# Optimization experiments

Measured on AMD Instinct MI355X. Metric: run time of the kernel, lower is better.

The kernel has to match this reference:

```python
import jax, jax.numpy as jnp
import numpy as np
from jax.ops import segment_sum

N_NODES = 100000


def _add_self_loops(edge_index, n):
    loop = jnp.arange(n, dtype=edge_index.dtype)
    src = jnp.concatenate([edge_index[0], loop])
    dst = jnp.concatenate([edge_index[1], loop])
    return src, dst


def _gcn_conv(x, W, b, src, dst, n):
    # PyG GCNConv: h = X W; out[i] = sum_j norm(j,i) h[j] + b, with self-loops
    h = x @ W                                             # [N, out]
    deg = segment_sum(jnp.ones_like(src, dtype=x.dtype), dst, num_segments=n)
    dinv = jnp.where(deg > 0, jax.lax.rsqrt(deg), 0.0)    # deg^{-1/2}
    norm = dinv[src] * dinv[dst]                          # [E]
    msg = h[src] * norm[:, None]                          # gather + scale
    out = segment_sum(msg, dst, num_segments=n)           # scatter-add
    return out + b


def setup_inputs() -> dict:
    key = jax.random.key(0)
    ks = jax.random.split(key, 8)
    x = jax.random.normal(ks[0], (N_NODES, 128), dtype=jnp.float32)
    edge_index = jax.random.randint(ks[1], (2, 600000), 0, N_NODES, dtype=jnp.int64)
    s1 = 1.0 / np.sqrt(128); s2 = 1.0 / np.sqrt(64); s3 = 1.0 / np.sqrt(32)
    return {
        "x": x,
        "edge_index": edge_index,
        "W1": jax.random.uniform(ks[2], (128, 64), jnp.float32, -s1, s1),
        "b1": jnp.zeros((64,), jnp.float32),
        "W2": jax.random.uniform(ks[3], (64, 32), jnp.float32, -s2, s2),
        "b2": jnp.zeros((32,), jnp.float32),
        "Wc": jax.random.uniform(ks[4], (32, 1), jnp.float32, -s3, s3),
        "bc": jnp.zeros((1,), jnp.float32),
    }


def reference(x, edge_index, W1, b1, W2, b2, Wc, bc):
    n = x.shape[0]
    src, dst = _add_self_loops(edge_index, n)
    h = jax.nn.relu(_gcn_conv(x, W1, b1, src, dst, n))
    h = jax.nn.relu(_gcn_conv(h, W2, b2, src, dst, n))
    return h @ Wc + bc
```

## Files before the change

### kernel.cpp

```cpp
#include <hip/hip_runtime.h>


#define SCAN_THREADS 256
#define SCAN_PER_T   8
#define SCAN_TILE    (SCAN_THREADS * SCAN_PER_T)

__global__ __launch_bounds__(256) void count_kernel(const int* __restrict__ dst,
                                                    int* __restrict__ deg, int E) {
    int e = blockIdx.x * blockDim.x + threadIdx.x;
    if (e < E) atomicAdd(&deg[dst[e]], 1);
}

__global__ __launch_bounds__(SCAN_THREADS) void tile_reduce_kernel(const int* __restrict__ deg,
                                                                   int* __restrict__ bsum,
                                                                   int n) {
    __shared__ int s[SCAN_THREADS];
    int t = threadIdx.x;
    int gbase = blockIdx.x * SCAN_TILE + t * SCAN_PER_T;
    int local = 0;
#pragma unroll
    for (int k = 0; k < SCAN_PER_T; ++k) {
        int i = gbase + k;
        if (i < n) local += deg[i];
    }
    s[t] = local;
    __syncthreads();
    for (int off = SCAN_THREADS / 2; off > 0; off >>= 1) {
        if (t < off) s[t] += s[t + off];
        __syncthreads();
    }
    if (t == 0) bsum[blockIdx.x] = s[0];
}

__global__ __launch_bounds__(SCAN_THREADS) void scan_bsums_kernel(int* __restrict__ bsum,
                                                                  int* __restrict__ row_ptr,
                                                                  int nb, int n) {
    __shared__ int s[SCAN_THREADS];
    int t = threadIdx.x;
    s[t] = (t < nb) ? bsum[t] : 0;
    __syncthreads();
    for (int off = 1; off < SCAN_THREADS; off <<= 1) {
        int v = (t >= off) ? s[t - off] : 0;
        __syncthreads();
        s[t] += v;
        __syncthreads();
    }
    if (t < nb) bsum[t] = (t == 0) ? 0 : s[t - 1];
    if (t == 0) row_ptr[n] = s[nb - 1];
}

__global__ __launch_bounds__(SCAN_THREADS) void tile_apply_kernel(int* __restrict__ deg,
                                                                  const int* __restrict__ bsum,
                                                                  int* __restrict__ row_ptr,
                                                                  float* __restrict__ dinv,
                                                                  int n) {
    __shared__ int s[SCAN_THREADS];
    int t = threadIdx.x;
    int gbase = blockIdx.x * SCAN_TILE + t * SCAN_PER_T;

    int d[SCAN_PER_T];
    int inc[SCAN_PER_T];
    int run = 0;
#pragma unroll
    for (int k = 0; k < SCAN_PER_T; ++k) {
        int i = gbase + k;
        d[k] = (i < n) ? deg[i] : 0;
        run += d[k];
        inc[k] = run;
    }
    s[t] = run;
    __syncthreads();
    for (int off = 1; off < SCAN_THREADS; off <<= 1) {
        int v = (t >= off) ? s[t - off] : 0;
        __syncthreads();
        s[t] += v;
        __syncthreads();
    }
    int base = bsum[blockIdx.x] + ((t == 0) ? 0 : s[t - 1]);
#pragma unroll
    for (int k = 0; k < SCAN_PER_T; ++k) {
        int i = gbase + k;
        if (i < n) {
            int ex = base + inc[k] - d[k];
            row_ptr[i] = ex;
            deg[i] = ex;
            dinv[i] = rsqrtf((float)(d[k] + 1));
        }
    }
}

__global__ __launch_bounds__(256) void fill_kernel(const int* __restrict__ src,
                                                   const int* __restrict__ dst,
                                                   int* __restrict__ cursor,
                                                   int* __restrict__ col, int E) {
    int e = blockIdx.x * blockDim.x + threadIdx.x;
    if (e < E) {
        int pos = atomicAdd(&cursor[dst[e]], 1);
        col[pos] = src[e];
    }
}

template <int IN, int OUT>
__global__ __launch_bounds__(512) void gemm_kernel(const float* __restrict__ X,
                                                   const float* __restrict__ W,
                                                   float* __restrict__ H, int n) {
    constexpr int STRIP = OUT / 4;
    __shared__ float Ws[IN * OUT];
    for (int i = threadIdx.x; i < IN * OUT / 4; i += blockDim.x)
        ((float4*)Ws)[i] = ((const float4*)W)[i];
    __syncthreads();

    int t = blockIdx.x * blockDim.x + threadIdx.x;
    int node = t >> 2;
    int strip = (t & 3) * STRIP;
    if (node >= n) return;

    float acc[STRIP];
#pragma unroll
    for (int j = 0; j < STRIP; ++j) acc[j] = 0.f;

    const float* xr = X + (size_t)node * IN;
#pragma unroll 4
    for (int k = 0; k < IN; k += 4) {
        float4 xv = *(const float4*)(xr + k);
        const float* w0 = Ws + (k + 0) * OUT + strip;
        const float* w1 = Ws + (k + 1) * OUT + strip;
        const float* w2 = Ws + (k + 2) * OUT + strip;
        const float* w3 = Ws + (k + 3) * OUT + strip;
#pragma unroll
        for (int j = 0; j < STRIP; j += 4) {
            float4 a = *(const float4*)(w0 + j);
            float4 b = *(const float4*)(w1 + j);
            float4 c = *(const float4*)(w2 + j);
            float4 dd = *(const float4*)(w3 + j);
            acc[j + 0] += xv.x * a.x + xv.y * b.x + xv.z * c.x + xv.w * dd.x;
            acc[j + 1] += xv.x * a.y + xv.y * b.y + xv.z * c.y + xv.w * dd.y;
            acc[j + 2] += xv.x * a.z + xv.y * b.z + xv.z * c.z + xv.w * dd.z;
            acc[j + 3] += xv.x * a.w + xv.y * b.w + xv.z * c.w + xv.w * dd.w;
        }
    }

    float* hr = H + (size_t)node * OUT + strip;
#pragma unroll
    for (int j = 0; j < STRIP; j += 4)
        *(float4*)(hr + j) = make_float4(acc[j], acc[j + 1], acc[j + 2], acc[j + 3]);
}

template <int F>
__global__ __launch_bounds__(256) void agg_relu_kernel(const int* __restrict__ row_ptr,
                                                       const int* __restrict__ col,
                                                       const float* __restrict__ dinv,
                                                       const float* __restrict__ H,
                                                       const float* __restrict__ b,
                                                       float* __restrict__ OUT, int n) {
    constexpr int TPE = F / 4;
    int t = blockIdx.x * blockDim.x + threadIdx.x;
    int node = t / TPE;
    int c = t % TPE;
    if (node >= n) return;
    int rs = row_ptr[node], re = row_ptr[node + 1];
    float di = dinv[node];
    float4 acc = make_float4(0.f, 0.f, 0.f, 0.f);
    int e = rs;
    for (; e + 1 < re; e += 2) {
        int s0 = col[e], s1 = col[e + 1];
        float w0 = dinv[s0], w1 = dinv[s1];
        float4 v0 = *(const float4*)(H + (size_t)s0 * F + c * 4);
        float4 v1 = *(const float4*)(H + (size_t)s1 * F + c * 4);
        acc.x += w0 * v0.x + w1 * v1.x;
        acc.y += w0 * v0.y + w1 * v1.y;
        acc.z += w0 * v0.z + w1 * v1.z;
        acc.w += w0 * v0.w + w1 * v1.w;
    }
    if (e < re) {
        int s0 = col[e];
        float w0 = dinv[s0];
        float4 v0 = *(const float4*)(H + (size_t)s0 * F + c * 4);
        acc.x += w0 * v0.x; acc.y += w0 * v0.y;
        acc.z += w0 * v0.z; acc.w += w0 * v0.w;
    }
    float4 hs = *(const float4*)(H + (size_t)node * F + c * 4);
    float4 bb = *(const float4*)(b + c * 4);
    float d2 = di * di;
    float4 r;
    r.x = di * acc.x + d2 * hs.x + bb.x;
    r.y = di * acc.y + d2 * hs.y + bb.y;
    r.z = di * acc.z + d2 * hs.z + bb.z;
    r.w = di * acc.w + d2 * hs.w + bb.w;
    r.x = r.x > 0.f ? r.x : 0.f;
    r.y = r.y > 0.f ? r.y : 0.f;
    r.z = r.z > 0.f ? r.z : 0.f;
    r.w = r.w > 0.f ? r.w : 0.f;
    *(float4*)(OUT + (size_t)node * F + c * 4) = r;
}

__global__ __launch_bounds__(256) void agg_final_kernel(const int* __restrict__ row_ptr,
                                                        const int* __restrict__ col,
                                                        const float* __restrict__ dinv,
                                                        const float* __restrict__ H,
                                                        const float* __restrict__ b2,
                                                        const float* __restrict__ Wc,
                                                        const float* __restrict__ bc,
                                                        float* __restrict__ out, int n) {
    constexpr int F = 32, TPE = 8;
    int t = blockIdx.x * blockDim.x + threadIdx.x;
    int node = t / TPE;
    int c = t % TPE;
    if (node >= n) return;
    int rs = row_ptr[node], re = row_ptr[node + 1];
    float di = dinv[node];
    float4 acc = make_float4(0.f, 0.f, 0.f, 0.f);
    int e = rs;
    for (; e + 1 < re; e += 2) {
        int s0 = col[e], s1 = col[e + 1];
        float w0 = dinv[s0], w1 = dinv[s1];
        float4 v0 = *(const float4*)(H + (size_t)s0 * F + c * 4);
        float4 v1 = *(const float4*)(H + (size_t)s1 * F + c * 4);
        acc.x += w0 * v0.x + w1 * v1.x;
        acc.y += w0 * v0.y + w1 * v1.y;
        acc.z += w0 * v0.z + w1 * v1.z;
        acc.w += w0 * v0.w + w1 * v1.w;
    }
    if (e < re) {
        int s0 = col[e];
        float w0 = dinv[s0];
        float4 v0 = *(const float4*)(H + (size_t)s0 * F + c * 4);
        acc.x += w0 * v0.x; acc.y += w0 * v0.y;
        acc.z += w0 * v0.z; acc.w += w0 * v0.w;
    }
    float4 hs = *(const float4*)(H + (size_t)node * F + c * 4);
    float4 bb = *(const float4*)(b2 + c * 4);
    float4 wc = *(const float4*)(Wc + c * 4);
    float d2 = di * di;
    float4 r;
    r.x = di * acc.x + d2 * hs.x + bb.x;
    r.y = di * acc.y + d2 * hs.y + bb.y;
    r.z = di * acc.z + d2 * hs.z + bb.z;
    r.w = di * acc.w + d2 * hs.w + bb.w;
    float dot = (r.x > 0.f ? r.x : 0.f) * wc.x + (r.y > 0.f ? r.y : 0.f) * wc.y +
                (r.z > 0.f ? r.z : 0.f) * wc.z + (r.w > 0.f ? r.w : 0.f) * wc.w;
    dot += __shfl_xor(dot, 1, 8);
    dot += __shfl_xor(dot, 2, 8);
    dot += __shfl_xor(dot, 4, 8);
    if (c == 0) out[node] = dot + bc[0];
}

extern "C" void kernel_launch(void* const* d_in, const int* in_sizes, int n_in,
                              void* d_out, int out_size, void* d_ws, size_t ws_size,
                              hipStream_t stream) {
    const float* x  = (const float*)d_in[0];
    const int*   ei = (const int*)d_in[1];
    const float* W1 = (const float*)d_in[2];
    const float* b1 = (const float*)d_in[3];
    const float* W2 = (const float*)d_in[4];
    const float* b2 = (const float*)d_in[5];
    const float* Wc = (const float*)d_in[6];
    const float* bc = (const float*)d_in[7];
    float* out = (float*)d_out;

    const int n = in_sizes[0] / 128;
    const int E = in_sizes[1] / 2;

    const int* src = ei;
    const int* dst = ei + (size_t)E;

    const int nb = (n + SCAN_TILE - 1) / SCAN_TILE;

    float* dinv    = (float*)d_ws;
    int*   deg     = (int*)d_ws + n;
    int*   row_ptr = (int*)d_ws + 2 * (size_t)n;
    int*   col     = row_ptr + (n + 1);
    int*   bsum    = col + E;
    float* bufA    = (float*)(bsum + 256);
    float* bufB    = bufA + (size_t)n * 64;

    hipMemsetAsync(deg, 0, (size_t)n * 4, stream);
    count_kernel<<<(E + 255) / 256, 256, 0, stream>>>(dst, deg, E);
    tile_reduce_kernel<<<nb, SCAN_THREADS, 0, stream>>>(deg, bsum, n);
    scan_bsums_kernel<<<1, SCAN_THREADS, 0, stream>>>(bsum, row_ptr, nb, n);
    tile_apply_kernel<<<nb, SCAN_THREADS, 0, stream>>>(deg, bsum, row_ptr, dinv, n);
    fill_kernel<<<(E + 255) / 256, 256, 0, stream>>>(src, dst, deg, col, E);

    gemm_kernel<128, 64><<<(n * 4 + 511) / 512, 512, 0, stream>>>(x, W1, bufA, n);
    agg_relu_kernel<64><<<(n * 16 + 255) / 256, 256, 0, stream>>>(row_ptr, col, dinv,
                                                                  bufA, b1, bufB, n);
    gemm_kernel<64, 32><<<(n * 4 + 511) / 512, 512, 0, stream>>>(bufB, W2, bufA, n);
    agg_final_kernel<<<(n * 8 + 255) / 256, 256, 0, stream>>>(row_ptr, col, dinv,
                                                              bufA, b2, Wc, bc, out, n);
}
```

Baseline: 271.9 us.

## Restructure GEMM to stage X tiles in LDS and read W via uniform loads

```diff
diff --git a/kernel.cpp b/kernel.cpp
--- a/kernel.cpp
+++ b/kernel.cpp
@@ -101,49 +101,72 @@
 }
 
 template <int IN, int OUT>
-__global__ __launch_bounds__(512) void gemm_kernel(const float* __restrict__ X,
+__global__ __launch_bounds__(256) void gemm_kernel(const float* __restrict__ X,
                                                    const float* __restrict__ W,
                                                    float* __restrict__ H, int n) {
-    constexpr int STRIP = OUT / 4;
-    __shared__ float Ws[IN * OUT];
-    for (int i = threadIdx.x; i < IN * OUT / 4; i += blockDim.x)
-        ((float4*)Ws)[i] = ((const float4*)W)[i];
-    __syncthreads();
-
-    int t = blockIdx.x * blockDim.x + threadIdx.x;
-    int node = t >> 2;
-    int strip = (t & 3) * STRIP;
-    if (node >= n) return;
-
-    float acc[STRIP];
-#pragma unroll
-    for (int j = 0; j < STRIP; ++j) acc[j] = 0.f;
-
-    const float* xr = X + (size_t)node * IN;
-#pragma unroll 4
-    for (int k = 0; k < IN; k += 4) {
-        float4 xv = *(const float4*)(xr + k);
-        const float* w0 = Ws + (k + 0) * OUT + strip;
-        const float* w1 = Ws + (k + 1) * OUT + strip;
-        const float* w2 = Ws + (k + 2) * OUT + strip;
-        const float* w3 = Ws + (k + 3) * OUT + strip;
-#pragma unroll
-        for (int j = 0; j < STRIP; j += 4) {
-            float4 a = *(const float4*)(w0 + j);
-            float4 b = *(const float4*)(w1 + j);
-            float4 c = *(const float4*)(w2 + j);
-            float4 dd = *(const float4*)(w3 + j);
-            acc[j + 0] += xv.x * a.x + xv.y * b.x + xv.z * c.x + xv.w * dd.x;
-            acc[j + 1] += xv.x * a.y + xv.y * b.y + xv.z * c.y + xv.w * dd.y;
-            acc[j + 2] += xv.x * a.z + xv.y * b.z + xv.z * c.z + xv.w * dd.z;
-            acc[j + 3] += xv.x * a.w + xv.y * b.w + xv.z * c.w + xv.w * dd.w;
+    constexpr int NB = 128;
+    constexpr int KT = 32;
+    constexpr int STRIDE = KT + 1;
+    constexpr int JW = OUT / 2;
+    constexpr int NKT = IN / KT;
+    constexpr int NF4 = NB * KT / 4;
+
+    __shared__ float Xs[NB * STRIDE];
+
+    const int t = threadIdx.x;
+    const int wv = __builtin_amdgcn_readfirstlane(t >> 6);
+    const int lane = t & 63;
+    const int node0 = blockIdx.x * NB;
+    const int lnode = ((wv >> 1) << 6) + lane;
+    const int jbase = (wv & 1) * JW;
+    const int node = node0 + lnode;
+
+    float acc[JW];
+#pragma unroll
+    for (int j = 0; j < JW; ++j) acc[j] = 0.f;
+
+    for (int kt = 0; kt < NKT; ++kt) {
+        __syncthreads();
+        for (int f = t; f < NF4; f += 256) {
+            int nd = f >> 3;
+            int kq = f & 7;
+            float4 val = make_float4(0.f, 0.f, 0.f, 0.f);
+            if (node0 + nd < n)
+                val = *(const float4*)(X + (size_t)(node0 + nd) * IN + kt * KT + kq * 4);
+            float* p = Xs + nd * STRIDE + kq * 4;
+            p[0] = val.x; p[1] = val.y; p[2] = val.z; p[3] = val.w;
         }
-    }
-
-    float* hr = H + (size_t)node * OUT + strip;
-#pragma unroll
-    for (int j = 0; j < STRIP; j += 4)
-        *(float4*)(hr + j) = make_float4(acc[j], acc[j + 1], acc[j + 2], acc[j + 3]);
+        __syncthreads();
+
+        const float* xrow = Xs + lnode * STRIDE;
+#pragma unroll
+        for (int kq = 0; kq < KT; kq += 4) {
+            float x0 = xrow[kq + 0];
+            float x1 = xrow[kq + 1];
+            float x2 = xrow[kq + 2];
+            float x3 = xrow[kq + 3];
+            const float* wr = W + (size_t)(kt * KT + kq) * OUT + jbase;
+#pragma unroll
+            for (int jg = 0; jg < JW; jg += 4) {
+                float4 w0 = *(const float4*)(wr + 0 * OUT + jg);
+                float4 w1 = *(const float4*)(wr + 1 * OUT + jg);
+                float4 w2 = *(const float4*)(wr + 2 * OUT + jg);
+                float4 w3 = *(const float4*)(wr + 3 * OUT + jg);
+                acc[jg + 0] += x0 * w0.x + x1 * w1.x + x2 * w2.x + x3 * w3.x;
+                acc[jg + 1] += x0 * w0.y + x1 * w1.y + x2 * w2.y + x3 * w3.y;
+                acc[jg + 2] += x0 * w0.z + x1 * w1.z + x2 * w2.z + x3 * w3.z;
+                acc[jg + 3] += x0 * w0.w + x1 * w1.w + x2 * w2.w + x3 * w3.w;
+            }
+        }
+    }
+
+    if (node < n) {
+        float* hr = H + (size_t)node * OUT + jbase;
+#pragma unroll
+        for (int jg = 0; jg < JW; jg += 4)
+            *(float4*)(hr + jg) =
+                make_float4(acc[jg], acc[jg + 1], acc[jg + 2], acc[jg + 3]);
+    }
 }
 
 template <int F>
@@ -281,10 +304,12 @@
     tile_apply_kernel<<<nb, SCAN_THREADS, 0, stream>>>(deg, bsum, row_ptr, dinv, n);
     fill_kernel<<<(E + 255) / 256, 256, 0, stream>>>(src, dst, deg, col, E);
 
-    gemm_kernel<128, 64><<<(n * 4 + 511) / 512, 512, 0, stream>>>(x, W1, bufA, n);
+    const int gemm_grid = (n + 127) / 128;
+
+    gemm_kernel<128, 64><<<gemm_grid, 256, 0, stream>>>(x, W1, bufA, n);
     agg_relu_kernel<64><<<(n * 16 + 255) / 256, 256, 0, stream>>>(row_ptr, col, dinv,
                                                                   bufA, b1, bufB, n);
-    gemm_kernel<64, 32><<<(n * 4 + 511) / 512, 512, 0, stream>>>(bufB, W2, bufA, n);
+    gemm_kernel<64, 32><<<gemm_grid, 256, 0, stream>>>(bufB, W2, bufA, n);
     agg_final_kernel<<<(n * 8 + 255) / 256, 256, 0, stream>>>(row_ptr, col, dinv,
                                                               bufA, b2, Wc, bc, out, n);
 }
```

After: 275.7 us. Within noise of the previous version (+1.4%).

## Replace per-node GEMM with shared-memory tiled register-blocked GEMM

Applied to the files above, without the earlier changes.

```diff
diff --git a/kernel.cpp b/kernel.cpp
--- a/kernel.cpp
+++ b/kernel.cpp
@@ -100,50 +100,71 @@
     }
 }
 
-template <int IN, int OUT>
-__global__ __launch_bounds__(512) void gemm_kernel(const float* __restrict__ X,
-                                                   const float* __restrict__ W,
-                                                   float* __restrict__ H, int n) {
-    constexpr int STRIP = OUT / 4;
+template <int IN, int OUT, int BM, int TM, int TN>
+__global__ __launch_bounds__(256) void gemm_tiled(const float* __restrict__ X,
+                                                  const float* __restrict__ W,
+                                                  float* __restrict__ H, int n) {
+    constexpr int BK = 32;
+    constexpr int XST = BK + 1;
+    constexpr int NTX = OUT / TN;
+    constexpr int NF4 = BM * BK / 4;
+    static_assert(NTX * (BM / TM) == 256, "thread mapping");
+
     __shared__ float Ws[IN * OUT];
-    for (int i = threadIdx.x; i < IN * OUT / 4; i += blockDim.x)
+    __shared__ float Xs[BM * XST];
+
+    const int t = threadIdx.x;
+    for (int i = t; i < IN * OUT / 4; i += 256)
         ((float4*)Ws)[i] = ((const float4*)W)[i];
-    __syncthreads();
-
-    int t = blockIdx.x * blockDim.x + threadIdx.x;
-    int node = t >> 2;
-    int strip = (t & 3) * STRIP;
-    if (node >= n) return;
-
-    float acc[STRIP];
-#pragma unroll
-    for (int j = 0; j < STRIP; ++j) acc[j] = 0.f;
-
-    const float* xr = X + (size_t)node * IN;
+
+    const int node0 = blockIdx.x * BM;
+    const int tx = t % NTX;
+    const int ty = t / NTX;
+    const int row0 = ty * TM;
+    const int jb = tx * TN;
+
+    float acc[TM][TN];
+#pragma unroll
+    for (int i = 0; i < TM; ++i)
+#pragma unroll
+        for (int j = 0; j < TN; ++j) acc[i][j] = 0.f;
+
+    for (int kt = 0; kt < IN / BK; ++kt) {
+        __syncthreads();
+        for (int f = t; f < NF4; f += 256) {
+            int nd = f >> 3;
+            int kq = f & 7;
+            float4 val = make_float4(0.f, 0.f, 0.f, 0.f);
+            if (node0 + nd < n)
+                val = *(const float4*)(X + (size_t)(node0 + nd) * IN + kt * BK + kq * 4);
+            float* p = Xs + nd * XST + kq * 4;
+            p[0] = val.x; p[1] = val.y; p[2] = val.z; p[3] = val.w;
+        }
+        __syncthreads();
+
 #pragma unroll 4
-    for (int k = 0; k < IN; k += 4) {
-        float4 xv = *(const float4*)(xr + k);
-        const float* w0 = Ws + (k + 0) * OUT + strip;
-        const float* w1 = Ws + (k + 1) * OUT + strip;
-        const float* w2 = Ws + (k + 2) * OUT + strip;
-        const float* w3 = Ws + (k + 3) * OUT + strip;
-#pragma unroll
-        for (int j = 0; j < STRIP; j += 4) {
-            float4 a = *(const float4*)(w0 + j);
-            float4 b = *(const float4*)(w1 + j);
-            float4 c = *(const float4*)(w2 + j);
-            float4 dd = *(const float4*)(w3 + j);
-            acc[j + 0] += xv.x * a.x + xv.y * b.x + xv.z * c.x + xv.w * dd.x;
-            acc[j + 1] += xv.x * a.y + xv.y * b.y + xv.z * c.y + xv.w * dd.y;
-            acc[j + 2] += xv.x * a.z + xv.y * b.z + xv.z * c.z + xv.w * dd.z;
-            acc[j + 3] += xv.x * a.w + xv.y * b.w + xv.z * c.w + xv.w * dd.w;
+        for (int k = 0; k < BK; ++k) {
+            float xv[TM];
+#pragma unroll
+            for (int i = 0; i < TM; ++i) xv[i] = Xs[(row0 + i) * XST + k];
+            float4 wv = *(const float4*)(Ws + (size_t)(kt * BK + k) * OUT + jb);
+#pragma unroll
+            for (int i = 0; i < TM; ++i) {
+                acc[i][0] += xv[i] * wv.x;
+                acc[i][1] += xv[i] * wv.y;
+                acc[i][2] += xv[i] * wv.z;
+                acc[i][3] += xv[i] * wv.w;
+            }
         }
     }
 
-    float* hr = H + (size_t)node * OUT + strip;
-#pragma unroll
-    for (int j = 0; j < STRIP; j += 4)
-        *(float4*)(hr + j) = make_float4(acc[j], acc[j + 1], acc[j + 2], acc[j + 3]);
+#pragma unroll
+    for (int i = 0; i < TM; ++i) {
+        int node = node0 + row0 + i;
+        if (node < n)
+            *(float4*)(H + (size_t)node * OUT + jb) =
+                make_float4(acc[i][0], acc[i][1], acc[i][2], acc[i][3]);
+    }
 }
 
 template <int F>
@@ -281,10 +302,12 @@
     tile_apply_kernel<<<nb, SCAN_THREADS, 0, stream>>>(deg, bsum, row_ptr, dinv, n);
     fill_kernel<<<(E + 255) / 256, 256, 0, stream>>>(src, dst, deg, col, E);
 
-    gemm_kernel<128, 64><<<(n * 4 + 511) / 512, 512, 0, stream>>>(x, W1, bufA, n);
+    const int gemm_grid = (n + 127) / 128;
+
+    gemm_tiled<128, 64, 128, 8, 4><<<gemm_grid, 256, 0, stream>>>(x, W1, bufA, n);
     agg_relu_kernel<64><<<(n * 16 + 255) / 256, 256, 0, stream>>>(row_ptr, col, dinv,
                                                                   bufA, b1, bufB, n);
-    gemm_kernel<64, 32><<<(n * 4 + 511) / 512, 512, 0, stream>>>(bufB, W2, bufA, n);
+    gemm_tiled<64, 32, 128, 4, 4><<<gemm_grid, 256, 0, stream>>>(bufB, W2, bufA, n);
     agg_final_kernel<<<(n * 8 + 255) / 256, 256, 0, stream>>>(row_ptr, col, dinv,
                                                               bufA, b2, Wc, bc, out, n);
 }
```

New measurement: 268.9 us. Within noise of the previous version (-1.1%).
